# Optimization experiments

Measured on AMD Instinct MI355X. Metric: run time of the kernel, lower is better.

Reference implementation:

```python
import jax, jax.numpy as jnp
import numpy as np

N = 150000   # total nodes across batch
E = 2400000  # edges (avg degree 16)
F = 20       # netlsd feature dim
H = 32       # hidden_channels
G = 1000     # graphs in batch
K = 30       # sort-pool k
D_TOT = H * 3 + 1  # 97, concat latent dim


def setup_inputs() -> dict:
    key = jax.random.key(0)
    ks = jax.random.split(key, 20)
    s = lambda fan: 1.0 / np.sqrt(fan)
    inp = {
        "x": jax.random.normal(ks[0], (N, F), jnp.float32),
        "edge_index": jax.random.randint(ks[1], (2, E), 0, N),
        "batch": jnp.sort(jax.random.randint(ks[2], (N,), 0, G)),
        # GCN conv params: (20->32), (32->32), (32->32), (32->1)
        "W0": jax.random.normal(ks[3], (F, H), jnp.float32) * s(F),
        "b0": jnp.zeros((H,), jnp.float32),
        "W1": jax.random.normal(ks[4], (H, H), jnp.float32) * s(H),
        "b1": jnp.zeros((H,), jnp.float32),
        "W2": jax.random.normal(ks[5], (H, H), jnp.float32) * s(H),
        "b2": jnp.zeros((H,), jnp.float32),
        "W3": jax.random.normal(ks[6], (H, 1), jnp.float32) * s(H),
        "b3": jnp.zeros((1,), jnp.float32),
        # conv1d head: Conv1d(1,16,97,stride=97), Conv1d(16,32,5,stride=1)
        "conv1_w": jax.random.normal(ks[7], (16, 1, D_TOT), jnp.float32) * s(D_TOT),
        "conv1_b": jnp.zeros((16,), jnp.float32),
        "conv2_w": jax.random.normal(ks[8], (32, 16, 5), jnp.float32) * s(16 * 5),
        "conv2_b": jnp.zeros((32,), jnp.float32),
        # MLP([352, 32, 1]) (dropout inactive at inference)
        "mlp_w1": jax.random.normal(ks[9], (352, 32), jnp.float32) * s(352),
        "mlp_b1": jnp.zeros((32,), jnp.float32),
        "mlp_w2": jax.random.normal(ks[10], (32, 1), jnp.float32) * s(32),
        "mlp_b2": jnp.zeros((1,), jnp.float32),
    }
    return inp


def reference(x, edge_index, batch, W0, b0, W1, b1, W2, b2, W3, b3,
              conv1_w, conv1_b, conv2_w, conv2_b,
              mlp_w1, mlp_b1, mlp_w2, mlp_b2):
    n = x.shape[0]
    # add self-loops (GCNConv default)
    loop = jnp.arange(n)
    src = jnp.concatenate([edge_index[0], loop])
    dst = jnp.concatenate([edge_index[1], loop])
    deg = jax.ops.segment_sum(jnp.ones_like(src, x.dtype), dst, num_segments=n)
    dis = jax.lax.rsqrt(jnp.maximum(deg, 1.0))  # deg >= 1 with self-loops
    norm = dis[src] * dis[dst]  # [E+N]

    def gcn(h, W, b):
        m = (h @ W)[src] * norm[:, None]                      # gather + scale
        return jax.ops.segment_sum(m, dst, num_segments=n) + b  # scatter-add

    h = x
    xs = []
    for W, b in ((W0, b0), (W1, b1), (W2, b2), (W3, b3)):
        h = jnp.tanh(gcn(h, W, b))
        xs.append(h)
    feat = jnp.concatenate(xs, axis=-1)  # [N, 97]
    d = feat.shape[-1]

    # global_sort_pool: per-graph sort by last channel (desc), top-K, zero-pad
    last = feat[:, -1]
    order = jnp.lexsort((-last, batch))  # group by graph, desc within graph
    b_s = batch[order]
    f_s = feat[order]
    counts = jax.ops.segment_sum(jnp.ones_like(batch), batch, num_segments=G)
    starts = jnp.cumsum(counts) - counts  # exclusive prefix
    rank = jnp.arange(n) - starts[b_s]
    valid = rank < K
    pooled = jnp.zeros((G, K, d), feat.dtype).at[
        b_s, jnp.where(valid, rank, 0)
    ].add(jnp.where(valid[:, None], f_s, 0.0))  # [G, K, 97]

    seq = pooled.reshape(G, 1, K * d)  # [G, 1, 2910]
    dn = ('NCH', 'OIH', 'NCH')
    y = jax.lax.conv_general_dilated(seq, conv1_w, (d,), 'VALID',
                                     dimension_numbers=dn) + conv1_b[None, :, None]
    y = jax.nn.relu(y)  # [G, 16, 30]
    y = jax.lax.reduce_window(y, -jnp.inf, jax.lax.max,
                              (1, 1, 2), (1, 1, 2), 'VALID')  # [G, 16, 15]
    y = jax.lax.conv_general_dilated(y, conv2_w, (1,), 'VALID',
                                     dimension_numbers=dn) + conv2_b[None, :, None]
    y = jax.nn.relu(y).reshape(G, -1)  # [G, 352]
    y = jax.nn.relu(y @ mlp_w1 + mlp_b1)
    return y @ mlp_w2 + mlp_b2  # [G, 1]
```

## Files before the change

### kernel.cpp

```cpp
#include <hip/hip_runtime.h>
#include <math.h>

constexpr int D_TOT = 97;
constexpr int K_POOL = 30;
constexpr int BSHIFT = 10;
constexpr int BSIZE  = 1 << BSHIFT;
constexpr int MAXB   = 256;

__global__ __launch_bounds__(256) void k_bcount(const int* __restrict__ dst, int E,
                                                int* __restrict__ bucketcnt, int B) {
    __shared__ int h[MAXB];
    int t = threadIdx.x;
    for (int i = t; i < MAXB; i += 256) h[i] = 0;
    __syncthreads();
    int e0 = blockIdx.x * 4096;
    int cnt = min(4096, E - e0);
    if (cnt == 4096) {
        const int4* d4 = (const int4*)(dst + e0);
        for (int i = t; i < 1024; i += 256) {
            int4 v = d4[i];
            atomicAdd(&h[v.x >> BSHIFT], 1);
            atomicAdd(&h[v.y >> BSHIFT], 1);
            atomicAdd(&h[v.z >> BSHIFT], 1);
            atomicAdd(&h[v.w >> BSHIFT], 1);
        }
    } else {
        for (int i = t; i < cnt; i += 256)
            atomicAdd(&h[dst[e0 + i] >> BSHIFT], 1);
    }
    __syncthreads();
    for (int i = t; i < B; i += 256)
        if (h[i]) atomicAdd(&bucketcnt[i], h[i]);
}

__global__ void k_bscan_starts(const int* __restrict__ cnt, int* __restrict__ bstart,
                               int* __restrict__ bcursor, int B, int E,
                               const int* __restrict__ batch, int n, int G,
                               int* __restrict__ starts) {
    int t = threadIdx.x;
    if (blockIdx.x == 0) {
        __shared__ int s[MAXB];
        int mine = (t < B) ? cnt[t] : 0;
        s[t] = mine;
        __syncthreads();
        for (int off = 1; off < MAXB; off <<= 1) {
            int add = (t >= off) ? s[t - off] : 0;
            __syncthreads();
            s[t] += add;
            __syncthreads();
        }
        if (t < B) { int ex = s[t] - mine; bstart[t] = ex; bcursor[t] = ex; }
        if (t == 0) bstart[B] = E;
    } else {
        int g = (blockIdx.x - 1) * 256 + t;
        if (g > G) return;
        if (g == G) { starts[G] = n; return; }
        int lo = 0, hi = n;
        while (lo < hi) { int mid = (lo + hi) >> 1; if (batch[mid] < g) lo = mid + 1; else hi = mid; }
        starts[g] = lo;
    }
}

__global__ void k_t0(const float* __restrict__ x,
                     const float* __restrict__ W0,
                     float* __restrict__ t0, int n) {
    int t = blockIdx.x * blockDim.x + threadIdx.x;
    int i = t / 32, c = t % 32;
    if (i >= n) return;
    const float* xr = x + (size_t)i * 20;
    float a = 0.f;
#pragma unroll
    for (int f = 0; f < 20; ++f) a += xr[f] * W0[f * 32 + c];
    t0[(size_t)i * 32 + c] = a;
}

__global__ __launch_bounds__(256) void k_part(const int* __restrict__ src,
                                              const int* __restrict__ dst, int E, int B,
                                              int* __restrict__ bcursor,
                                              unsigned* __restrict__ bpk) {
    __shared__ int4 s_src4[1024];
    __shared__ int4 s_dst4[1024];
    __shared__ int hist[MAXB];
    __shared__ int base[MAXB];
    int* s_src = (int*)s_src4;
    int* s_dst = (int*)s_dst4;
    int t = threadIdx.x;
    int e0 = blockIdx.x * 4096;
    int cnt = min(4096, E - e0);
    for (int i = t; i < MAXB; i += 256) hist[i] = 0;
    __syncthreads();
    if (cnt == 4096) {
        const int4* sv4 = (const int4*)(src + e0);
        const int4* dv4 = (const int4*)(dst + e0);
        for (int i = t; i < 1024; i += 256) {
            int4 a = sv4[i];
            int4 b = dv4[i];
            s_src4[i] = a;
            s_dst4[i] = b;
            atomicAdd(&hist[b.x >> BSHIFT], 1);
            atomicAdd(&hist[b.y >> BSHIFT], 1);
            atomicAdd(&hist[b.z >> BSHIFT], 1);
            atomicAdd(&hist[b.w >> BSHIFT], 1);
        }
    } else {
        for (int i = t; i < cnt; i += 256) {
            int d = dst[e0 + i];
            s_src[i] = src[e0 + i];
            s_dst[i] = d;
            atomicAdd(&hist[d >> BSHIFT], 1);
        }
    }
    __syncthreads();
    for (int i = t; i < B; i += 256) {
        int hh = hist[i];
        base[i] = hh ? atomicAdd(&bcursor[i], hh) : 0;
        hist[i] = 0;
    }
    __syncthreads();
    for (int i = t; i < cnt; i += 256) {
        int d = s_dst[i];
        int b = d >> BSHIFT;
        int off = atomicAdd(&hist[b], 1);
        bpk[base[b] + off] = ((unsigned)(d & (BSIZE - 1)) << 18) | (unsigned)s_src[i];
    }
}

__global__ __launch_bounds__(512) void k_fill3(const unsigned* __restrict__ bpk,
                                               const int* __restrict__ bstart,
                                               int n, int B,
                                               int* __restrict__ deg,
                                               int* __restrict__ rowstart,
                                               float* __restrict__ dis,
                                               int* __restrict__ ssrc,
                                               const float4* __restrict__ t04,
                                               float4* __restrict__ gA4) {
    __shared__ int cnt[BSIZE];
    __shared__ int s512[512];
    __shared__ float sdis[BSIZE];
    int b = blockIdx.x;
    int t = threadIdx.x;
    int s0 = bstart[b], s1 = bstart[b + 1];

    for (int i = t; i < BSIZE; i += 512) cnt[i] = 0;
    __syncthreads();
    for (int i = s0 + t; i < s1; i += 512)
        atomicAdd(&cnt[bpk[i] >> 18], 1);
    __syncthreads();

    int c0 = cnt[2 * t], c1 = cnt[2 * t + 1];
    int tot = c0 + c1;
    s512[t] = tot;
    __syncthreads();
    for (int off = 1; off < 512; off <<= 1) {
        int add = (t >= off) ? s512[t - off] : 0;
        __syncthreads();
        s512[t] += add;
        __syncthreads();
    }
    int g0 = s0 + s512[t] - tot;
    int p0 = g0, p1 = g0 + c0;

    float d0 = rsqrtf((float)(c0 + 1)), d1 = rsqrtf((float)(c1 + 1));
    sdis[2 * t] = d0; sdis[2 * t + 1] = d1;

    int node0 = (b << BSHIFT) + 2 * t;
    if (node0 + 0 < n) { rowstart[node0 + 0] = p0; deg[node0 + 0] = c0; dis[node0 + 0] = d0; }
    if (node0 + 1 < n) { rowstart[node0 + 1] = p1; deg[node0 + 1] = c1; dis[node0 + 1] = d1; }

    cnt[2 * t] = p0; cnt[2 * t + 1] = p1;
    __syncthreads();

    for (int i = s0 + t; i < s1; i += 512) {
        unsigned pk = bpk[i];
        int pos = atomicAdd(&cnt[pk >> 18], 1);
        ssrc[pos] = (int)(pk & 0x3FFFFu);
    }

    int basei = b << BSHIFT;
    int nn = min(BSIZE, n - basei);
    for (int q = t; q < nn * 8; q += 512) {
        int il = q >> 3;
        float4 v = t04[(size_t)basei * 8 + q];
        float s = sdis[il];
        gA4[(size_t)basei * 8 + q] = make_float4(s * v.x, s * v.y, s * v.z, s * v.w);
    }
}

template<int MODE>
__global__ __launch_bounds__(256) void k_gather32f(
    const int* __restrict__ rowstart, const int* __restrict__ deg,
    const int* __restrict__ ssrc, const float4* __restrict__ g4,
    const float* __restrict__ dis, const float* __restrict__ bias,
    const float* __restrict__ Wn,
    float* __restrict__ feat, int off,
    float* __restrict__ gnext, int n)
{
    __shared__ float hs[32][33];
    __shared__ float wsm[32 * 32];
    int t = blockIdx.x * 256 + threadIdx.x;
    int i = t >> 3, p = t & 7;
    bool valid = (i < n);

    if (MODE == 0) {
        for (int q = threadIdx.x; q < 1024; q += 256) wsm[q] = Wn[q];
    }

    float h0 = 0.f, h1 = 0.f, h2 = 0.f, h3 = 0.f;
    float sc = 0.f;
    if (valid) {
        int r0 = rowstart[i], d = deg[i];
        float4 acc = g4[(size_t)i * 8 + p];
        int j = 0;
        for (; j + 4 <= d; j += 4) {
            int s0 = ssrc[r0 + j + 0];
            int s1 = ssrc[r0 + j + 1];
            int s2 = ssrc[r0 + j + 2];
            int s3 = ssrc[r0 + j + 3];
            float4 v0 = g4[(size_t)s0 * 8 + p];
            float4 v1 = g4[(size_t)s1 * 8 + p];
            float4 v2 = g4[(size_t)s2 * 8 + p];
            float4 v3 = g4[(size_t)s3 * 8 + p];
            acc.x += (v0.x + v1.x) + (v2.x + v3.x);
            acc.y += (v0.y + v1.y) + (v2.y + v3.y);
            acc.z += (v0.z + v1.z) + (v2.z + v3.z);
            acc.w += (v0.w + v1.w) + (v2.w + v3.w);
        }
        for (; j < d; ++j) {
            int s = ssrc[r0 + j];
            float4 v = g4[(size_t)s * 8 + p];
            acc.x += v.x; acc.y += v.y; acc.z += v.z; acc.w += v.w;
        }
        sc = dis[i];
        h0 = tanhf(sc * acc.x + bias[p * 4 + 0]);
        h1 = tanhf(sc * acc.y + bias[p * 4 + 1]);
        h2 = tanhf(sc * acc.z + bias[p * 4 + 2]);
        h3 = tanhf(sc * acc.w + bias[p * 4 + 3]);
        float* fr = feat + (size_t)i * D_TOT + off + p * 4;
        fr[0] = h0; fr[1] = h1; fr[2] = h2; fr[3] = h3;
    }

    int nl = threadIdx.x >> 3;
    hs[nl][p * 4 + 0] = h0;
    hs[nl][p * 4 + 1] = h1;
    hs[nl][p * 4 + 2] = h2;
    hs[nl][p * 4 + 3] = h3;
    __syncthreads();

    if (MODE == 0) {
        if (valid) {
            float a0 = 0.f, a1 = 0.f, a2 = 0.f, a3 = 0.f;
            const float* hr = hs[nl];
            int c0 = p * 4;
#pragma unroll
            for (int f = 0; f < 32; ++f) {
                float hv = hr[f];
                const float* wr = &wsm[f * 32 + c0];
                a0 += hv * wr[0];
                a1 += hv * wr[1];
                a2 += hv * wr[2];
                a3 += hv * wr[3];
            }
            float4* gn = (float4*)gnext;
            gn[(size_t)i * 8 + p] = make_float4(sc * a0, sc * a1, sc * a2, sc * a3);
        }
    } else {
        if (valid && p == 0) {
            float a = 0.f;
            const float* hr = hs[nl];
#pragma unroll
            for (int f = 0; f < 32; ++f) a += hr[f] * Wn[f];
            gnext[i] = sc * a;
        }
    }
}

constexpr int SORTN = 512;

__global__ __launch_bounds__(256) void k_cnn(
    const float* __restrict__ feat,
    const int* __restrict__ starts,
    const int* __restrict__ rowstart, const int* __restrict__ deg,
    const int* __restrict__ ssrc, const float* __restrict__ g1,
    const float* __restrict__ dis, const float* __restrict__ b3,
    const float* __restrict__ c1w, const float* __restrict__ c1b,
    const float* __restrict__ c2w, const float* __restrict__ c2b,
    const float* __restrict__ m1w, const float* __restrict__ m1b,
    const float* __restrict__ m2w, const float* __restrict__ m2b,
    float* __restrict__ out)
{
    int g = blockIdx.x;
    int tid = threadIdx.x;

    __shared__ unsigned long long keys[SORTN];
    __shared__ float vals[SORTN];
    __shared__ float pooled[K_POOL][D_TOT];
    __shared__ float y[16][K_POOL];
    __shared__ float z[16][15];
    __shared__ float u[352];
    __shared__ float pm[256];
    __shared__ float hid[32];

    int start = starts[g];
    int cnt = starts[g + 1] - start;
    if (cnt > SORTN) cnt = SORTN;
    int kk = cnt < K_POOL ? cnt : K_POOL;
    float bias3 = b3[0];

    for (int il = tid; il < cnt; il += 256) {
        int i = start + il;
        int r0 = rowstart[i], d = deg[i];
        float acc = g1[i];
        for (int j = 0; j < d; ++j) acc += g1[ssrc[r0 + j]];
        vals[il] = tanhf(dis[i] * acc + bias3);
    }
    __syncthreads();

    int SN = (cnt <= 256) ? 256 : SORTN;

    for (int i = tid; i < SN; i += 256) {
        unsigned long long kv;
        if (i < cnt) {
            float v = vals[i];
            unsigned uo = __float_as_uint(v);
            uo ^= (unsigned)((int)uo >> 31) | 0x80000000u;
            kv = ((unsigned long long)(~uo) << 32) | (unsigned)i;
        } else {
            kv = 0xFFFFFFFFFFFFFFFFull;
        }
        keys[i] = kv;
    }
    __syncthreads();

    for (int sz = 2; sz <= SN; sz <<= 1) {
        for (int j = sz >> 1; j > 0; j >>= 1) {
            for (int q = tid; q < SN; q += 256) {
                int l = q ^ j;
                if (l > q) {
                    bool asc = ((q & sz) == 0);
                    unsigned long long a = keys[q], bb = keys[l];
                    if ((a > bb) == asc) { keys[q] = bb; keys[l] = a; }
                }
            }
            __syncthreads();
        }
    }

    float* pf = &pooled[0][0];
    for (int t = tid; t < K_POOL * D_TOT; t += 256) pf[t] = 0.f;
    __syncthreads();
    for (int t = tid; t < kk * 96; t += 256) {
        int r = t / 96, c = t - r * 96;
        int idx = (int)(keys[r] & 0xFFFFFFFFull);
        pooled[r][c] = feat[(size_t)(start + idx) * D_TOT + c];
    }
    for (int r = tid; r < kk; r += 256) {
        int idx = (int)(keys[r] & 0xFFFFFFFFull);
        pooled[r][96] = vals[idx];
    }
    __syncthreads();

    for (int t = tid; t < 16 * K_POOL; t += 256) {
        int o = t / K_POOL, p = t - o * K_POOL;
        float a = c1b[o];
        const float* w = c1w + o * D_TOT;
        const float* pr = &pooled[p][0];
#pragma unroll 1
        for (int c = 0; c < D_TOT; ++c) a += pr[c] * w[c];
        y[o][p] = fmaxf(a, 0.f);
    }
    __syncthreads();

    for (int t = tid; t < 16 * 15; t += 256) {
        int o = t / 15, p = t - o * 15;
        z[o][p] = fmaxf(y[o][2 * p], y[o][2 * p + 1]);
    }
    __syncthreads();

    for (int t = tid; t < 32 * 11; t += 256) {
        int q = t / 11, p = t - q * 11;
        float a = c2b[q];
        const float* w = c2w + q * 16 * 5;
#pragma unroll 1
        for (int c = 0; c < 16; ++c) {
#pragma unroll
            for (int j = 0; j < 5; ++j) a += z[c][p + j] * w[c * 5 + j];
        }
        u[t] = fmaxf(a, 0.f);
    }
    __syncthreads();

    {
        int grp = tid >> 5, o = tid & 31;
        float a = 0.f;
        int i0 = grp * 44;
#pragma unroll 1
        for (int i = i0; i < i0 + 44; ++i) a += u[i] * m1w[i * 32 + o];
        pm[tid] = a;
    }
    __syncthreads();
    if (tid < 32) {
        float a = m1b[tid];
#pragma unroll
        for (int gg = 0; gg < 8; ++gg) a += pm[tid + 32 * gg];
        hid[tid] = fmaxf(a, 0.f);
    }
    __syncthreads();

    if (tid == 0) {
        float a = m2b[0];
#pragma unroll
        for (int m = 0; m < 32; ++m) a += hid[m] * m2w[m];
        out[g] = a;
    }
}

extern "C" void kernel_launch(void* const* d_in, const int* in_sizes, int n_in,
                              void* d_out, int out_size, void* d_ws, size_t ws_size,
                              hipStream_t stream) {
    const float* x    = (const float*)d_in[0];
    const int*   ei   = (const int*)d_in[1];
    const int*   batch= (const int*)d_in[2];
    const float* W0   = (const float*)d_in[3];
    const float* b0   = (const float*)d_in[4];
    const float* W1   = (const float*)d_in[5];
    const float* b1   = (const float*)d_in[6];
    const float* W2   = (const float*)d_in[7];
    const float* b2   = (const float*)d_in[8];
    const float* W3   = (const float*)d_in[9];
    const float* b3   = (const float*)d_in[10];
    const float* c1w  = (const float*)d_in[11];
    const float* c1b  = (const float*)d_in[12];
    const float* c2w  = (const float*)d_in[13];
    const float* c2b  = (const float*)d_in[14];
    const float* m1w  = (const float*)d_in[15];
    const float* m1b  = (const float*)d_in[16];
    const float* m2w  = (const float*)d_in[17];
    const float* m2b  = (const float*)d_in[18];

    const int n = in_sizes[0] / 20;
    const int E = in_sizes[1] / 2;
    const int G = out_size;
    const int* srcv = ei;
    const int* dstv = ei + E;
    const int B = (n + BSIZE - 1) >> BSHIFT;
    const int nE4 = (E + 4095) / 4096;

    char* ws = (char*)d_ws;
    float* feat    = (float*)ws;  ws += (size_t)n * D_TOT * sizeof(float);
    float* gA      = (float*)ws;  ws += (size_t)n * 32 * sizeof(float);
    float* gB      = (float*)ws;  ws += (size_t)n * 32 * sizeof(float);
    float* t0      = (float*)ws;  ws += (size_t)n * 32 * sizeof(float);
    int*   ssrc    = (int*)ws;    ws += (size_t)E * sizeof(int);
    unsigned* bpk  = (unsigned*)ws; ws += (size_t)E * sizeof(unsigned);
    int*   rowstart= (int*)ws;    ws += (size_t)n * sizeof(int);
    int*   deg     = (int*)ws;    ws += (size_t)n * sizeof(int);
    float* dis     = (float*)ws;  ws += (size_t)n * sizeof(float);
    int*   startsb = (int*)ws;    ws += (size_t)(G + 1) * sizeof(int);
    int*   bucketcnt=(int*)ws;    ws += (size_t)MAXB * sizeof(int);
    int*   bstart  = (int*)ws;    ws += (size_t)(MAXB + 1) * sizeof(int);
    int*   bcursor = (int*)ws;    ws += (size_t)MAXB * sizeof(int);
    float* g1      = (float*)bpk;

    hipMemsetAsync(bucketcnt, 0, (size_t)MAXB * sizeof(int), stream);

    k_t0<<<(n * 32 + 255) / 256, 256, 0, stream>>>(x, W0, t0, n);

    k_bcount<<<nE4, 256, 0, stream>>>(dstv, E, bucketcnt, B);
    const int nSB = (G + 1 + 255) / 256;
    k_bscan_starts<<<1 + nSB, 256, 0, stream>>>(bucketcnt, bstart, bcursor, B, E,
                                                batch, n, G, startsb);
    k_part<<<nE4, 256, 0, stream>>>(srcv, dstv, E, B, bcursor, bpk);
    k_fill3<<<B, 512, 0, stream>>>(bpk, bstart, n, B, deg, rowstart, dis, ssrc,
                                   (const float4*)t0, (float4*)gA);

    const int nb8 = (n * 8 + 255) / 256;
    k_gather32f<0><<<nb8, 256, 0, stream>>>(rowstart, deg, ssrc, (const float4*)gA, dis, b0, W1, feat, 0, gB, n);
    k_gather32f<0><<<nb8, 256, 0, stream>>>(rowstart, deg, ssrc, (const float4*)gB, dis, b1, W2, feat, 32, gA, n);
    k_gather32f<1><<<nb8, 256, 0, stream>>>(rowstart, deg, ssrc, (const float4*)gA, dis, b2, W3, feat, 64, g1, n);

    k_cnn<<<G, 256, 0, stream>>>(feat, startsb, rowstart, deg, ssrc, g1, dis, b3,
                                 c1w, c1b, c2w, c2b, m1w, m1b, m2w, m2b,
                                 (float*)d_out);
}
```

Before: 449.9 us.

## Split gather features into 8 slice-major slabs and separate transform kernels

Stores the scaled GCN features in a slice-major layout, eight slabs of float4 per node, so each gather block touches only one 16-byte slice of every node. The goal is a smaller random-access working set per block, which should improve cache hit rates. The dense 32x32 transform is moved out of the gather into its own kernel that re-reads the layer output from feat. k_t0 now runs after the fill and folds the dis scaling in itself. The trade-off is three extra kernel launches and extra feat reads and slab writes, in exchange for gathers with better locality.

```diff
diff --git a/kernel.cpp b/kernel.cpp
--- a/kernel.cpp
+++ b/kernel.cpp
@@ -61,19 +61,6 @@
     }
 }
 
-__global__ void k_t0(const float* __restrict__ x,
-                     const float* __restrict__ W0,
-                     float* __restrict__ t0, int n) {
-    int t = blockIdx.x * blockDim.x + threadIdx.x;
-    int i = t / 32, c = t % 32;
-    if (i >= n) return;
-    const float* xr = x + (size_t)i * 20;
-    float a = 0.f;
-#pragma unroll
-    for (int f = 0; f < 20; ++f) a += xr[f] * W0[f * 32 + c];
-    t0[(size_t)i * 32 + c] = a;
-}
-
 __global__ __launch_bounds__(256) void k_part(const int* __restrict__ src,
                                               const int* __restrict__ dst, int E, int B,
                                               int* __restrict__ bcursor,
@@ -131,12 +118,9 @@
                                                int* __restrict__ deg,
                                                int* __restrict__ rowstart,
                                                float* __restrict__ dis,
-                                               int* __restrict__ ssrc,
-                                               const float4* __restrict__ t04,
-                                               float4* __restrict__ gA4) {
+                                               int* __restrict__ ssrc) {
     __shared__ int cnt[BSIZE];
     __shared__ int s512[512];
-    __shared__ float sdis[BSIZE];
     int b = blockIdx.x;
     int t = threadIdx.x;
     int s0 = bstart[b], s1 = bstart[b + 1];
@@ -161,7 +145,6 @@
     int p0 = g0, p1 = g0 + c0;
 
     float d0 = rsqrtf((float)(c0 + 1)), d1 = rsqrtf((float)(c1 + 1));
-    sdis[2 * t] = d0; sdis[2 * t + 1] = d1;
 
     int node0 = (b << BSHIFT) + 2 * t;
     if (node0 + 0 < n) { rowstart[node0 + 0] = p0; deg[node0 + 0] = c0; dis[node0 + 0] = d0; }
@@ -175,82 +158,98 @@
         int pos = atomicAdd(&cnt[pk >> 18], 1);
         ssrc[pos] = (int)(pk & 0x3FFFFu);
     }
-
-    int basei = b << BSHIFT;
-    int nn = min(BSIZE, n - basei);
-    for (int q = t; q < nn * 8; q += 512) {
-        int il = q >> 3;
-        float4 v = t04[(size_t)basei * 8 + q];
-        float s = sdis[il];
-        gA4[(size_t)basei * 8 + q] = make_float4(s * v.x, s * v.y, s * v.z, s * v.w);
-    }
+}
+
+__global__ void k_t0(const float* __restrict__ x,
+                     const float* __restrict__ W0,
+                     const float* __restrict__ dis,
+                     float4* __restrict__ slab, int n) {
+    int t = blockIdx.x * blockDim.x + threadIdx.x;
+    if (t >= n * 8) return;
+    int p = t / n, i = t - p * n;
+    const float* xr = x + (size_t)i * 20;
+    int c0 = p * 4;
+    float a0 = 0.f, a1 = 0.f, a2 = 0.f, a3 = 0.f;
+#pragma unroll
+    for (int f = 0; f < 20; ++f) {
+        float xv = xr[f];
+        const float* wr = &W0[f * 32 + c0];
+        a0 += xv * wr[0];
+        a1 += xv * wr[1];
+        a2 += xv * wr[2];
+        a3 += xv * wr[3];
+    }
+    float sc = dis[i];
+    slab[t] = make_float4(sc * a0, sc * a1, sc * a2, sc * a3);
+}
+
+__global__ __launch_bounds__(256) void k_gatherT(
+    const int* __restrict__ rowstart, const int* __restrict__ deg,
+    const int* __restrict__ ssrc, const float4* __restrict__ slab,
+    const float* __restrict__ dis, const float* __restrict__ bias,
+    float* __restrict__ feat, int off, int n)
+{
+    int slice = blockIdx.x & 7;
+    int i = (blockIdx.x >> 3) * 256 + threadIdx.x;
+    if (i >= n) return;
+    const float4* sl = slab + (size_t)slice * n;
+    int r0 = rowstart[i], d = deg[i];
+    float4 acc = sl[i];
+    int j = 0;
+    for (; j + 4 <= d; j += 4) {
+        int s0 = ssrc[r0 + j + 0];
+        int s1 = ssrc[r0 + j + 1];
+        int s2 = ssrc[r0 + j + 2];
+        int s3 = ssrc[r0 + j + 3];
+        float4 v0 = sl[s0];
+        float4 v1 = sl[s1];
+        float4 v2 = sl[s2];
+        float4 v3 = sl[s3];
+        acc.x += (v0.x + v1.x) + (v2.x + v3.x);
+        acc.y += (v0.y + v1.y) + (v2.y + v3.y);
+        acc.z += (v0.z + v1.z) + (v2.z + v3.z);
+        acc.w += (v0.w + v1.w) + (v2.w + v3.w);
+    }
+    for (; j < d; ++j) {
+        float4 v = sl[ssrc[r0 + j]];
+        acc.x += v.x; acc.y += v.y; acc.z += v.z; acc.w += v.w;
+    }
+    float sc = dis[i];
+    float* fr = feat + (size_t)i * D_TOT + off + slice * 4;
+    fr[0] = tanhf(sc * acc.x + bias[slice * 4 + 0]);
+    fr[1] = tanhf(sc * acc.y + bias[slice * 4 + 1]);
+    fr[2] = tanhf(sc * acc.z + bias[slice * 4 + 2]);
+    fr[3] = tanhf(sc * acc.w + bias[slice * 4 + 3]);
 }
 
 template<int MODE>
-__global__ __launch_bounds__(256) void k_gather32f(
-    const int* __restrict__ rowstart, const int* __restrict__ deg,
-    const int* __restrict__ ssrc, const float4* __restrict__ g4,
-    const float* __restrict__ dis, const float* __restrict__ bias,
-    const float* __restrict__ Wn,
-    float* __restrict__ feat, int off,
-    float* __restrict__ gnext, int n)
+__global__ __launch_bounds__(256) void k_trans(
+    const float* __restrict__ feat, int off,
+    const float* __restrict__ dis, const float* __restrict__ Wn,
+    float4* __restrict__ slabNext, float* __restrict__ g1, int n)
 {
     __shared__ float hs[32][33];
     __shared__ float wsm[32 * 32];
-    int t = blockIdx.x * 256 + threadIdx.x;
-    int i = t >> 3, p = t & 7;
-    bool valid = (i < n);
+    int base = blockIdx.x * 32;
+    int tid = threadIdx.x;
 
     if (MODE == 0) {
-        for (int q = threadIdx.x; q < 1024; q += 256) wsm[q] = Wn[q];
-    }
-
-    float h0 = 0.f, h1 = 0.f, h2 = 0.f, h3 = 0.f;
-    float sc = 0.f;
-    if (valid) {
-        int r0 = rowstart[i], d = deg[i];
-        float4 acc = g4[(size_t)i * 8 + p];
-        int j = 0;
-        for (; j + 4 <= d; j += 4) {
-            int s0 = ssrc[r0 + j + 0];
-            int s1 = ssrc[r0 + j + 1];
-            int s2 = ssrc[r0 + j + 2];
-            int s3 = ssrc[r0 + j + 3];
-            float4 v0 = g4[(size_t)s0 * 8 + p];
-            float4 v1 = g4[(size_t)s1 * 8 + p];
-            float4 v2 = g4[(size_t)s2 * 8 + p];
-            float4 v3 = g4[(size_t)s3 * 8 + p];
-            acc.x += (v0.x + v1.x) + (v2.x + v3.x);
-            acc.y += (v0.y + v1.y) + (v2.y + v3.y);
-            acc.z += (v0.z + v1.z) + (v2.z + v3.z);
-            acc.w += (v0.w + v1.w) + (v2.w + v3.w);
-        }
-        for (; j < d; ++j) {
-            int s = ssrc[r0 + j];
-            float4 v = g4[(size_t)s * 8 + p];
-            acc.x += v.x; acc.y += v.y; acc.z += v.z; acc.w += v.w;
-        }
-        sc = dis[i];
-        h0 = tanhf(sc * acc.x + bias[p * 4 + 0]);
-        h1 = tanhf(sc * acc.y + bias[p * 4 + 1]);
-        h2 = tanhf(sc * acc.z + bias[p * 4 + 2]);
-        h3 = tanhf(sc * acc.w + bias[p * 4 + 3]);
-        float* fr = feat + (size_t)i * D_TOT + off + p * 4;
-        fr[0] = h0; fr[1] = h1; fr[2] = h2; fr[3] = h3;
-    }
-
-    int nl = threadIdx.x >> 3;
-    hs[nl][p * 4 + 0] = h0;
-    hs[nl][p * 4 + 1] = h1;
-    hs[nl][p * 4 + 2] = h2;
-    hs[nl][p * 4 + 3] = h3;
+        for (int q = tid; q < 1024; q += 256) wsm[q] = Wn[q];
+    }
+    for (int q = tid; q < 1024; q += 256) {
+        int il = q >> 5, c = q & 31;
+        int i = base + il;
+        hs[il][c] = (i < n) ? feat[(size_t)i * D_TOT + off + c] : 0.f;
+    }
     __syncthreads();
 
     if (MODE == 0) {
-        if (valid) {
+        int p = tid >> 5, il = tid & 31;
+        int i = base + il;
+        if (i < n) {
+            const float* hr = hs[il];
+            int c0 = p * 4;
             float a0 = 0.f, a1 = 0.f, a2 = 0.f, a3 = 0.f;
-            const float* hr = hs[nl];
-            int c0 = p * 4;
 #pragma unroll
             for (int f = 0; f < 32; ++f) {
                 float hv = hr[f];
@@ -260,16 +259,19 @@
                 a2 += hv * wr[2];
                 a3 += hv * wr[3];
             }
-            float4* gn = (float4*)gnext;
-            gn[(size_t)i * 8 + p] = make_float4(sc * a0, sc * a1, sc * a2, sc * a3);
+            float sc = dis[i];
+            slabNext[(size_t)p * n + i] = make_float4(sc * a0, sc * a1, sc * a2, sc * a3);
         }
     } else {
-        if (valid && p == 0) {
-            float a = 0.f;
-            const float* hr = hs[nl];
-#pragma unroll
-            for (int f = 0; f < 32; ++f) a += hr[f] * Wn[f];
-            gnext[i] = sc * a;
+        if (tid < 32) {
+            int i = base + tid;
+            if (i < n) {
+                const float* hr = hs[tid];
+                float a = 0.f;
+#pragma unroll
+                for (int f = 0; f < 32; ++f) a += hr[f] * Wn[f];
+                g1[i] = dis[i] * a;
+            }
         }
     }
 }
@@ -447,9 +449,8 @@
 
     char* ws = (char*)d_ws;
     float* feat    = (float*)ws;  ws += (size_t)n * D_TOT * sizeof(float);
-    float* gA      = (float*)ws;  ws += (size_t)n * 32 * sizeof(float);
-    float* gB      = (float*)ws;  ws += (size_t)n * 32 * sizeof(float);
-    float* t0      = (float*)ws;  ws += (size_t)n * 32 * sizeof(float);
+    float* slabA   = (float*)ws;  ws += (size_t)n * 32 * sizeof(float);
+    float* slabB   = (float*)ws;  ws += (size_t)n * 32 * sizeof(float);
     int*   ssrc    = (int*)ws;    ws += (size_t)E * sizeof(int);
     unsigned* bpk  = (unsigned*)ws; ws += (size_t)E * sizeof(unsigned);
     int*   rowstart= (int*)ws;    ws += (size_t)n * sizeof(int);
@@ -463,20 +464,24 @@
 
     hipMemsetAsync(bucketcnt, 0, (size_t)MAXB * sizeof(int), stream);
 
-    k_t0<<<(n * 32 + 255) / 256, 256, 0, stream>>>(x, W0, t0, n);
-
     k_bcount<<<nE4, 256, 0, stream>>>(dstv, E, bucketcnt, B);
     const int nSB = (G + 1 + 255) / 256;
     k_bscan_starts<<<1 + nSB, 256, 0, stream>>>(bucketcnt, bstart, bcursor, B, E,
                                                 batch, n, G, startsb);
     k_part<<<nE4, 256, 0, stream>>>(srcv, dstv, E, B, bcursor, bpk);
-    k_fill3<<<B, 512, 0, stream>>>(bpk, bstart, n, B, deg, rowstart, dis, ssrc,
-                                   (const float4*)t0, (float4*)gA);
-
-    const int nb8 = (n * 8 + 255) / 256;
-    k_gather32f<0><<<nb8, 256, 0, stream>>>(rowstart, deg, ssrc, (const float4*)gA, dis, b0, W1, feat, 0, gB, n);
-    k_gather32f<0><<<nb8, 256, 0, stream>>>(rowstart, deg, ssrc, (const float4*)gB, dis, b1, W2, feat, 32, gA, n);
-    k_gather32f<1><<<nb8, 256, 0, stream>>>(rowstart, deg, ssrc, (const float4*)gA, dis, b2, W3, feat, 64, g1, n);
+    k_fill3<<<B, 512, 0, stream>>>(bpk, bstart, n, B, deg, rowstart, dis, ssrc);
+
+    k_t0<<<(n * 8 + 255) / 256, 256, 0, stream>>>(x, W0, dis, (float4*)slabA, n);
+
+    const int nchunk = (n + 255) / 256;
+    const int gridT = nchunk * 8;
+    const int ntr = (n + 31) / 32;
+    k_gatherT<<<gridT, 256, 0, stream>>>(rowstart, deg, ssrc, (const float4*)slabA, dis, b0, feat, 0, n);
+    k_trans<0><<<ntr, 256, 0, stream>>>(feat, 0, dis, W1, (float4*)slabB, nullptr, n);
+    k_gatherT<<<gridT, 256, 0, stream>>>(rowstart, deg, ssrc, (const float4*)slabB, dis, b1, feat, 32, n);
+    k_trans<0><<<ntr, 256, 0, stream>>>(feat, 32, dis, W2, (float4*)slabA, nullptr, n);
+    k_gatherT<<<gridT, 256, 0, stream>>>(rowstart, deg, ssrc, (const float4*)slabA, dis, b2, feat, 64, n);
+    k_trans<1><<<ntr, 256, 0, stream>>>(feat, 64, dis, W3, nullptr, g1, n);
 
     k_cnn<<<G, 256, 0, stream>>>(feat, startsb, rowstart, deg, ssrc, g1, dis, b3,
                                  c1w, c1b, c2w, c2b, m1w, m1b, m2w, m2b,
```

Measured after the change: 653.5 us. 45.2% more time.

## Halve CSR bucket size and fold degree scaling into the first-layer transform

Applied to the files above, without the earlier changes.

Buckets now hold 512 destination nodes instead of 1024, so the partition stage has twice as many buckets (about 293 fill blocks) and each fill thread handles one node instead of two. The first-layer x·W0 kernel now runs after the fill kernel and multiplies by dis directly. This removes the t0 buffer and the extra read and write pass that scaled it inside the fill kernel. The cost is a serialized dependency: the transform can no longer overlap the CSR build, and k_bcount and k_part now use 512-entry shared histograms with more global atomics on bucket counters.

```diff
diff --git a/kernel.cpp b/kernel.cpp
--- a/kernel.cpp
+++ b/kernel.cpp
@@ -3,9 +3,9 @@
 
 constexpr int D_TOT = 97;
 constexpr int K_POOL = 30;
-constexpr int BSHIFT = 10;
+constexpr int BSHIFT = 9;
 constexpr int BSIZE  = 1 << BSHIFT;
-constexpr int MAXB   = 256;
+constexpr int MAXB   = 512;
 
 __global__ __launch_bounds__(256) void k_bcount(const int* __restrict__ dst, int E,
                                                 int* __restrict__ bucketcnt, int B) {
@@ -33,10 +33,11 @@
         if (h[i]) atomicAdd(&bucketcnt[i], h[i]);
 }
 
-__global__ void k_bscan_starts(const int* __restrict__ cnt, int* __restrict__ bstart,
-                               int* __restrict__ bcursor, int B, int E,
-                               const int* __restrict__ batch, int n, int G,
-                               int* __restrict__ starts) {
+__global__ __launch_bounds__(512) void k_bscan_starts(
+        const int* __restrict__ cnt, int* __restrict__ bstart,
+        int* __restrict__ bcursor, int B, int E,
+        const int* __restrict__ batch, int n, int G,
+        int* __restrict__ starts) {
     int t = threadIdx.x;
     if (blockIdx.x == 0) {
         __shared__ int s[MAXB];
@@ -52,26 +53,13 @@
         if (t < B) { int ex = s[t] - mine; bstart[t] = ex; bcursor[t] = ex; }
         if (t == 0) bstart[B] = E;
     } else {
-        int g = (blockIdx.x - 1) * 256 + t;
+        int g = (blockIdx.x - 1) * 512 + t;
         if (g > G) return;
         if (g == G) { starts[G] = n; return; }
         int lo = 0, hi = n;
         while (lo < hi) { int mid = (lo + hi) >> 1; if (batch[mid] < g) lo = mid + 1; else hi = mid; }
         starts[g] = lo;
     }
-}
-
-__global__ void k_t0(const float* __restrict__ x,
-                     const float* __restrict__ W0,
-                     float* __restrict__ t0, int n) {
-    int t = blockIdx.x * blockDim.x + threadIdx.x;
-    int i = t / 32, c = t % 32;
-    if (i >= n) return;
-    const float* xr = x + (size_t)i * 20;
-    float a = 0.f;
-#pragma unroll
-    for (int f = 0; f < 20; ++f) a += xr[f] * W0[f * 32 + c];
-    t0[(size_t)i * 32 + c] = a;
 }
 
 __global__ __launch_bounds__(256) void k_part(const int* __restrict__ src,
@@ -131,25 +119,21 @@
                                                int* __restrict__ deg,
                                                int* __restrict__ rowstart,
                                                float* __restrict__ dis,
-                                               int* __restrict__ ssrc,
-                                               const float4* __restrict__ t04,
-                                               float4* __restrict__ gA4) {
+                                               int* __restrict__ ssrc) {
     __shared__ int cnt[BSIZE];
     __shared__ int s512[512];
-    __shared__ float sdis[BSIZE];
     int b = blockIdx.x;
     int t = threadIdx.x;
     int s0 = bstart[b], s1 = bstart[b + 1];
 
-    for (int i = t; i < BSIZE; i += 512) cnt[i] = 0;
+    cnt[t] = 0;
     __syncthreads();
     for (int i = s0 + t; i < s1; i += 512)
         atomicAdd(&cnt[bpk[i] >> 18], 1);
     __syncthreads();
 
-    int c0 = cnt[2 * t], c1 = cnt[2 * t + 1];
-    int tot = c0 + c1;
-    s512[t] = tot;
+    int c0 = cnt[t];
+    s512[t] = c0;
     __syncthreads();
     for (int off = 1; off < 512; off <<= 1) {
         int add = (t >= off) ? s512[t - off] : 0;
@@ -157,17 +141,15 @@
         s512[t] += add;
         __syncthreads();
     }
-    int g0 = s0 + s512[t] - tot;
-    int p0 = g0, p1 = g0 + c0;
-
-    float d0 = rsqrtf((float)(c0 + 1)), d1 = rsqrtf((float)(c1 + 1));
-    sdis[2 * t] = d0; sdis[2 * t + 1] = d1;
-
-    int node0 = (b << BSHIFT) + 2 * t;
-    if (node0 + 0 < n) { rowstart[node0 + 0] = p0; deg[node0 + 0] = c0; dis[node0 + 0] = d0; }
-    if (node0 + 1 < n) { rowstart[node0 + 1] = p1; deg[node0 + 1] = c1; dis[node0 + 1] = d1; }
-
-    cnt[2 * t] = p0; cnt[2 * t + 1] = p1;
+    int p0 = s0 + s512[t] - c0;
+
+    int node0 = (b << BSHIFT) + t;
+    if (node0 < n) {
+        rowstart[node0] = p0;
+        deg[node0] = c0;
+        dis[node0] = rsqrtf((float)(c0 + 1));
+    }
+    cnt[t] = p0;
     __syncthreads();
 
     for (int i = s0 + t; i < s1; i += 512) {
@@ -175,15 +157,20 @@
         int pos = atomicAdd(&cnt[pk >> 18], 1);
         ssrc[pos] = (int)(pk & 0x3FFFFu);
     }
-
-    int basei = b << BSHIFT;
-    int nn = min(BSIZE, n - basei);
-    for (int q = t; q < nn * 8; q += 512) {
-        int il = q >> 3;
-        float4 v = t04[(size_t)basei * 8 + q];
-        float s = sdis[il];
-        gA4[(size_t)basei * 8 + q] = make_float4(s * v.x, s * v.y, s * v.z, s * v.w);
-    }
+}
+
+__global__ void k_t0(const float* __restrict__ x,
+                     const float* __restrict__ W0,
+                     const float* __restrict__ dis,
+                     float* __restrict__ g, int n) {
+    int t = blockIdx.x * blockDim.x + threadIdx.x;
+    int i = t / 32, c = t % 32;
+    if (i >= n) return;
+    const float* xr = x + (size_t)i * 20;
+    float a = 0.f;
+#pragma unroll
+    for (int f = 0; f < 20; ++f) a += xr[f] * W0[f * 32 + c];
+    g[(size_t)i * 32 + c] = dis[i] * a;
 }
 
 template<int MODE>
@@ -449,7 +436,6 @@
     float* feat    = (float*)ws;  ws += (size_t)n * D_TOT * sizeof(float);
     float* gA      = (float*)ws;  ws += (size_t)n * 32 * sizeof(float);
     float* gB      = (float*)ws;  ws += (size_t)n * 32 * sizeof(float);
-    float* t0      = (float*)ws;  ws += (size_t)n * 32 * sizeof(float);
     int*   ssrc    = (int*)ws;    ws += (size_t)E * sizeof(int);
     unsigned* bpk  = (unsigned*)ws; ws += (size_t)E * sizeof(unsigned);
     int*   rowstart= (int*)ws;    ws += (size_t)n * sizeof(int);
@@ -463,15 +449,14 @@
 
     hipMemsetAsync(bucketcnt, 0, (size_t)MAXB * sizeof(int), stream);
 
-    k_t0<<<(n * 32 + 255) / 256, 256, 0, stream>>>(x, W0, t0, n);
-
     k_bcount<<<nE4, 256, 0, stream>>>(dstv, E, bucketcnt, B);
-    const int nSB = (G + 1 + 255) / 256;
-    k_bscan_starts<<<1 + nSB, 256, 0, stream>>>(bucketcnt, bstart, bcursor, B, E,
+    const int nSB = (G + 1 + 511) / 512;
+    k_bscan_starts<<<1 + nSB, 512, 0, stream>>>(bucketcnt, bstart, bcursor, B, E,
                                                 batch, n, G, startsb);
     k_part<<<nE4, 256, 0, stream>>>(srcv, dstv, E, B, bcursor, bpk);
-    k_fill3<<<B, 512, 0, stream>>>(bpk, bstart, n, B, deg, rowstart, dis, ssrc,
-                                   (const float4*)t0, (float4*)gA);
+    k_fill3<<<B, 512, 0, stream>>>(bpk, bstart, n, B, deg, rowstart, dis, ssrc);
+
+    k_t0<<<(n * 32 + 255) / 256, 256, 0, stream>>>(x, W0, dis, gA, n);
 
     const int nb8 = (n * 8 + 255) / 256;
     k_gather32f<0><<<nb8, 256, 0, stream>>>(rowstart, deg, ssrc, (const float4*)gA, dis, b0, W1, feat, 0, gB, n);
```

New measurement: 441.4 us. About the same (-1.9%).
